# Kernel tuning notes

Measured on AMD Instinct MI355X. Metric: run time of the kernel, lower is better.

## Reference

```python
import jax, jax.numpy as jnp
import numpy as np

LN_EPS = 1e-5  # torch LayerNorm default
MODES = 4


def setup_inputs() -> dict:
    key = jax.random.key(0)
    ks = jax.random.split(key, 5)
    B, S, H = 4, 4096, 1024
    nh, dk = 16, H // 16
    scale = 1.0 / (H * H)
    # frequency mode selection: random shuffle of range(S//2), take 4, sorted (seeded for determinism)
    rng = np.random.default_rng(0)
    index = jnp.asarray(np.sort(rng.permutation(S // 2)[:MODES]).astype(np.int32))
    return {
        "x": jax.random.normal(ks[0], (B, S, H), dtype=jnp.float32),
        "Wq": jax.random.normal(ks[1], (H, H), dtype=jnp.float32) * np.sqrt(2.0 / (H + dk)),
        "bq": jnp.zeros((H,), dtype=jnp.float32),
        "wr": scale * jax.random.uniform(ks[2], (nh, dk, dk, MODES), dtype=jnp.float32),
        "wi": scale * jax.random.uniform(ks[3], (nh, dk, dk, MODES), dtype=jnp.float32),
        "gamma": jnp.ones((H,), dtype=jnp.float32),
        "beta": jnp.zeros((H,), dtype=jnp.float32),
        "index": index,
    }


def reference(x, Wq, bq, wr, wi, gamma, beta, index):
    B, S, H = x.shape
    nh, dk = wr.shape[0], wr.shape[1]
    # q projection and head split: (B,S,H) -> (B,S,nh,dk) -> (B,nh,dk,S)
    q = (x @ Wq.T + bq).reshape(B, S, nh, dk).transpose(0, 2, 3, 1)
    x_ft = jnp.fft.rfft(q, axis=-1)                 # (B,nh,dk,S//2+1) complex
    xm = x_ft[..., index]                           # gather selected modes: (B,nh,dk,M)
    w = wr + 1j * wi                                # (nh,dk,dk,M) complex
    ym = jnp.einsum('bhim,hiom->bhom', xm, w)       # per-mode complex matmul
    # faithful: results written at slots 0..M-1 of out_ft (loop writes out_ft[...,wi])
    out_ft = jnp.zeros((B, nh, dk, S // 2 + 1), dtype=ym.dtype).at[..., :ym.shape[-1]].set(ym)
    x_if = jnp.fft.irfft(out_ft, n=S, axis=-1)      # (B,nh,dk,S) real
    # faithful permute(0,3,2,1).view: flattens as dk-major over heads
    out = x_if.transpose(0, 3, 2, 1).reshape(B, S, H)
    # dropout is identity in eval mode
    y = out + x
    mu = jnp.mean(y, axis=-1, keepdims=True)
    var = jnp.var(y, axis=-1, keepdims=True)
    return (y - mu) * jax.lax.rsqrt(var + LN_EPS) * gamma + beta
```

## Files before the change

kernel.cpp:

```cpp
#include <hip/hip_runtime.h>
#include <math.h>

#define BB 4
#define SS 4096
#define HH 1024
#define NH 16
#define DK 64
#define NMODES 4
#define TWO_PI 6.28318530717958647692f

__global__ __launch_bounds__(512) void kA_dft(const float* __restrict__ x,
                                              const int* __restrict__ index,
                                              float* __restrict__ Gp) {
    __shared__ float tab[1024 * 8];
    __shared__ float red[8][16][33];
    int t   = threadIdx.x;
    int bid = blockIdx.x;
    int cb  = bid & 15;
    int sq  = (bid >> 4) & 3;
    int b   = bid >> 6;

    int k0 = index[0], k1 = index[1], k2 = index[2], k3 = index[3];
    for (int u = t; u < 4096; u += 512) {
        int sl = u >> 2, m = u & 3;
        int k  = (m == 0) ? k0 : (m == 1) ? k1 : (m == 2) ? k2 : k3;
        int sv = sq * 1024 + sl;
        int r  = (k * sv) & (SS - 1);
        float ang = (float)r * (TWO_PI / (float)SS);
        float sn, cs;
        sincosf(ang, &sn, &cs);
        tab[sl * 8 + m * 2]     = cs;
        tab[sl * 8 + m * 2 + 1] = sn;
    }
    __syncthreads();

    int c4 = t & 15, srow = t >> 4;
    int c0 = cb * 64 + c4 * 4;
    float acc[4][8];
    #pragma unroll
    for (int e = 0; e < 4; ++e)
        #pragma unroll
        for (int q = 0; q < 8; ++q) acc[e][q] = 0.f;

    const float* xp = x + ((size_t)(b * SS + sq * 1024 + srow)) * HH + c0;
    #pragma unroll 8
    for (int pass = 0; pass < 32; ++pass) {
        float4 xv = *(const float4*)(xp + (size_t)pass * 32 * HH);
        int sl = pass * 32 + srow;
        float4 t0 = *(const float4*)&tab[sl * 8];
        float4 t1 = *(const float4*)&tab[sl * 8 + 4];
        float xe;
        #pragma unroll
        for (int e = 0; e < 4; ++e) {
            xe = (e == 0) ? xv.x : (e == 1) ? xv.y : (e == 2) ? xv.z : xv.w;
            acc[e][0] += xe * t0.x;  acc[e][1] -= xe * t0.y;
            acc[e][2] += xe * t0.z;  acc[e][3] -= xe * t0.w;
            acc[e][4] += xe * t1.x;  acc[e][5] -= xe * t1.y;
            acc[e][6] += xe * t1.z;  acc[e][7] -= xe * t1.w;
        }
    }
    #pragma unroll
    for (int e = 0; e < 4; ++e)
        #pragma unroll
        for (int q = 0; q < 8; ++q) {
            acc[e][q] += __shfl_xor(acc[e][q], 16);
            acc[e][q] += __shfl_xor(acc[e][q], 32);
        }
    int w = t >> 6, lane = t & 63;
    if (lane < 16) {
        #pragma unroll
        for (int e = 0; e < 4; ++e)
            #pragma unroll
            for (int q = 0; q < 8; ++q)
                red[w][lane][e * 8 + q] = acc[e][q];
    }
    __syncthreads();
    {
        int q = t >> 6, oc = t & 63;
        float s = 0.f;
        #pragma unroll
        for (int w2 = 0; w2 < 8; ++w2)
            s += red[w2][oc >> 2][(oc & 3) * 8 + q];
        Gp[((size_t)((b * 4 + sq) * 8 + q)) * HH + cb * 64 + oc] = s;
    }
}

__global__ __launch_bounds__(512) void kBC(const float* __restrict__ Gp,
                                           const float* __restrict__ Wq,
                                           const float* __restrict__ bq,
                                           const int* __restrict__ index,
                                           const float* __restrict__ wr,
                                           const float* __restrict__ wi,
                                           float* __restrict__ CF) {
    __shared__ float Gs[8 * HH];
    __shared__ float xs[DK * 8];
    __shared__ float red[8][DK][9];
    int t = threadIdx.x;
    int h = blockIdx.x & 15;
    int b = blockIdx.x >> 4;

    {
        const float4* g0 = (const float4*)(Gp + (size_t)(b * 4 + 0) * 8 * HH);
        const float4* g1 = (const float4*)(Gp + (size_t)(b * 4 + 1) * 8 * HH);
        const float4* g2 = (const float4*)(Gp + (size_t)(b * 4 + 2) * 8 * HH);
        const float4* g3 = (const float4*)(Gp + (size_t)(b * 4 + 3) * 8 * HH);
        float4* gd = (float4*)Gs;
        for (int u = t; u < 2 * HH; u += 512) {
            float4 a = g0[u], b2 = g1[u], c = g2[u], d = g3[u];
            gd[u] = make_float4(a.x + b2.x + c.x + d.x,
                                a.y + b2.y + c.y + d.y,
                                a.z + b2.z + c.z + d.z,
                                a.w + b2.w + c.w + d.w);
        }
    }
    __syncthreads();

    {
        int cl = t >> 3, jq = t & 7;
        int c = h * DK + cl;
        float acc[8] = {0.f,0.f,0.f,0.f,0.f,0.f,0.f,0.f};
        for (int j0 = jq * 4; j0 < HH; j0 += 32) {
            float4 wv = *(const float4*)&Wq[(size_t)c * HH + j0];
            #pragma unroll
            for (int q = 0; q < 8; ++q) {
                float4 gv = *(const float4*)&Gs[q * HH + j0];
                acc[q] += wv.x * gv.x + wv.y * gv.y + wv.z * gv.z + wv.w * gv.w;
            }
        }
        #pragma unroll
        for (int q = 0; q < 8; ++q) {
            acc[q] += __shfl_xor(acc[q], 1);
            acc[q] += __shfl_xor(acc[q], 2);
            acc[q] += __shfl_xor(acc[q], 4);
        }
        if (jq == 0) {
            float bias = bq[c];
            #pragma unroll
            for (int m = 0; m < NMODES; ++m)
                if (index[m] == 0) acc[2 * m] += bias * (float)SS;
            #pragma unroll
            for (int q = 0; q < 8; ++q) xs[cl * 8 + q] = acc[q];
        }
    }
    __syncthreads();

    {
        int o = t & 63, iq = t >> 6;
        float re[4] = {0.f,0.f,0.f,0.f}, im[4] = {0.f,0.f,0.f,0.f};
        #pragma unroll
        for (int ii = 0; ii < 8; ++ii) {
            int i = iq * 8 + ii;
            float4 wrv = *(const float4*)&wr[(((size_t)(h * DK + i)) * DK + o) * 4];
            float4 wiv = *(const float4*)&wi[(((size_t)(h * DK + i)) * DK + o) * 4];
            float xr, xi;
            xr = xs[i * 8 + 0]; xi = xs[i * 8 + 1];
            re[0] += xr * wrv.x - xi * wiv.x;  im[0] += xr * wiv.x + xi * wrv.x;
            xr = xs[i * 8 + 2]; xi = xs[i * 8 + 3];
            re[1] += xr * wrv.y - xi * wiv.y;  im[1] += xr * wiv.y + xi * wrv.y;
            xr = xs[i * 8 + 4]; xi = xs[i * 8 + 5];
            re[2] += xr * wrv.z - xi * wiv.z;  im[2] += xr * wiv.z + xi * wrv.z;
            xr = xs[i * 8 + 6]; xi = xs[i * 8 + 7];
            re[3] += xr * wrv.w - xi * wiv.w;  im[3] += xr * wiv.w + xi * wrv.w;
        }
        #pragma unroll
        for (int m = 0; m < 4; ++m) {
            red[iq][o][2 * m]     = re[m];
            red[iq][o][2 * m + 1] = im[m];
        }
        __syncthreads();
        if (iq == 0) {
            float rr[8];
            #pragma unroll
            for (int q = 0; q < 8; ++q) {
                float s = 0.f;
                #pragma unroll
                for (int g = 0; g < 8; ++g) s += red[g][o][q];
                rr[q] = s;
            }
            int co = o * NH + h;
            const float inv = 1.0f / (float)SS;
            float* cp = CF + ((size_t)(b * HH + co)) * 8;
            cp[0] =  rr[0] * inv;
            cp[1] =  2.0f * rr[2] * inv;
            cp[2] = -2.0f * rr[3] * inv;
            cp[3] =  2.0f * rr[4] * inv;
            cp[4] = -2.0f * rr[5] * inv;
            cp[5] =  2.0f * rr[6] * inv;
            cp[6] = -2.0f * rr[7] * inv;
            cp[7] =  0.0f;
        }
    }
}

#define KD_ROWS 8
__global__ __launch_bounds__(256) void kD_out(const float* __restrict__ x,
                                              const float* __restrict__ CF,
                                              const float* __restrict__ gamma,
                                              const float* __restrict__ beta,
                                              float* __restrict__ out) {
    __shared__ float red[4][KD_ROWS][2];
    int t  = threadIdx.x;
    int b  = blockIdx.x >> 9;
    int s0 = (blockIdx.x & 511) * KD_ROWS;
    int c0 = t * 4;

    float myc, mys;
    {
        float ang = (float)(s0 + (t & 7)) * (TWO_PI / (float)SS);
        sincosf(ang, &mys, &myc);
    }

    const float* cp = CF + (size_t)b * HH * 8 + (size_t)c0 * 8;
    float4 cfa[8];
    #pragma unroll
    for (int e = 0; e < 4; ++e) {
        cfa[2 * e]     = *(const float4*)(cp + e * 8);
        cfa[2 * e + 1] = *(const float4*)(cp + e * 8 + 4);
    }
    float4 g4 = *(const float4*)&gamma[c0];
    float4 b4 = *(const float4*)&beta[c0];
    int w = t >> 6, lane = t & 63;

    float4 yv[KD_ROWS];
    #pragma unroll
    for (int r = 0; r < KD_ROWS; ++r) {
        int s = s0 + r;
        yv[r] = *(const float4*)&x[((size_t)(b * SS + s)) * HH + c0];
    }
    float sm[KD_ROWS], sq[KD_ROWS];
    #pragma unroll
    for (int r = 0; r < KD_ROWS; ++r) {
        float c1 = __shfl(myc, r), s1 = __shfl(mys, r);
        float c2 = c1 * c1 - s1 * s1, s2 = 2.f * s1 * c1;
        float c3 = c2 * c1 - s2 * s1, s3 = s2 * c1 + c2 * s1;
        float ye[4];
        #pragma unroll
        for (int e = 0; e < 4; ++e) {
            float xe = (e == 0) ? yv[r].x : (e == 1) ? yv[r].y
                     : (e == 2) ? yv[r].z : yv[r].w;
            float4 A = cfa[2 * e], Bv = cfa[2 * e + 1];
            ye[e] = xe + A.x + A.y * c1 + A.z * s1 + A.w * c2
                       + Bv.x * s2 + Bv.y * c3 + Bv.z * s3;
        }
        yv[r] = make_float4(ye[0], ye[1], ye[2], ye[3]);
        sm[r] = ye[0] + ye[1] + ye[2] + ye[3];
        sq[r] = ye[0]*ye[0] + ye[1]*ye[1] + ye[2]*ye[2] + ye[3]*ye[3];
    }
    #pragma unroll
    for (int off = 1; off < 64; off <<= 1) {
        #pragma unroll
        for (int r = 0; r < KD_ROWS; ++r) {
            sm[r] += __shfl_xor(sm[r], off);
            sq[r] += __shfl_xor(sq[r], off);
        }
    }
    if (lane == 0) {
        #pragma unroll
        for (int r = 0; r < KD_ROWS; ++r) {
            red[w][r][0] = sm[r];
            red[w][r][1] = sq[r];
        }
    }
    __syncthreads();
    #pragma unroll
    for (int r = 0; r < KD_ROWS; ++r) {
        int s = s0 + r;
        float tot  = red[0][r][0] + red[1][r][0] + red[2][r][0] + red[3][r][0];
        float totq = red[0][r][1] + red[1][r][1] + red[2][r][1] + red[3][r][1];
        float mean = tot * (1.0f / (float)HH);
        float var  = totq * (1.0f / (float)HH) - mean * mean;
        float rs = rsqrtf(var + 1e-5f);
        float4 o4;
        o4.x = (yv[r].x - mean) * rs * g4.x + b4.x;
        o4.y = (yv[r].y - mean) * rs * g4.y + b4.y;
        o4.z = (yv[r].z - mean) * rs * g4.z + b4.z;
        o4.w = (yv[r].w - mean) * rs * g4.w + b4.w;
        *(float4*)&out[((size_t)(b * SS + s)) * HH + c0] = o4;
    }
}

extern "C" void kernel_launch(void* const* d_in, const int* in_sizes, int n_in,
                              void* d_out, int out_size, void* d_ws, size_t ws_size,
                              hipStream_t stream) {
    const float* x     = (const float*)d_in[0];
    const float* Wq    = (const float*)d_in[1];
    const float* bq    = (const float*)d_in[2];
    const float* wr    = (const float*)d_in[3];
    const float* wi    = (const float*)d_in[4];
    const float* gamma = (const float*)d_in[5];
    const float* beta  = (const float*)d_in[6];
    const int*   index = (const int*)d_in[7];
    float* out = (float*)d_out;
    float* ws  = (float*)d_ws;

    const size_t nGp = (size_t)BB * 4 * 8 * HH;
    const size_t nCF = (size_t)BB * HH * 8;

    float *Gp, *CFb;
    if (ws_size >= (nGp + nCF) * sizeof(float)) {
        Gp  = ws;
        CFb = ws + nGp;
    } else {
        Gp  = out;
        CFb = ws;
    }

    hipLaunchKernelGGL(kA_dft, dim3(BB * 64), dim3(512), 0, stream, x, index, Gp);
    hipLaunchKernelGGL(kBC,    dim3(BB * NH), dim3(512), 0, stream,
                       Gp, Wq, bq, index, wr, wi, CFb);
    hipLaunchKernelGGL(kD_out, dim3(BB * (SS / KD_ROWS)), dim3(256), 0, stream,
                       x, CFb, gamma, beta, out);
}
```

Before: 60.54 us.

## Split DFT reduction into many sequence chunks with partial-sum planes, reduce in kBC

The first kernel now runs one block per 32-row sequence chunk, and each thread owns four full columns. It writes per-chunk partial DFT sums into eight planes instead of doing an intra-block shuffle and shared-memory reduction. kBC then sums the 128 partials per batch when it loads Gs. The output kernel hoists its x loads earlier and uses nontemporal stores. This trades a larger partial-sum buffer (16 MB written then read) and a heavier reduction in the 64-block kBC for removing the in-block reductions and spreading the DFT over more blocks.

```diff
diff --git a/kernel.cpp b/kernel.cpp
--- a/kernel.cpp
+++ b/kernel.cpp
@@ -7,24 +7,25 @@
 #define NH 16
 #define DK 64
 #define NMODES 4
+#define NSB 128
+#define SCHUNK (SS/NSB)
+#define PPLANE ((size_t)BB * NSB * HH)
 #define TWO_PI 6.28318530717958647692f
 
-__global__ __launch_bounds__(512) void kA_dft(const float* __restrict__ x,
+typedef float nfloat4 __attribute__((ext_vector_type(4)));
+
+__global__ __launch_bounds__(256) void kA_dft(const float* __restrict__ x,
                                               const int* __restrict__ index,
-                                              float* __restrict__ Gp) {
-    __shared__ float tab[1024 * 8];
-    __shared__ float red[8][16][33];
-    int t   = threadIdx.x;
-    int bid = blockIdx.x;
-    int cb  = bid & 15;
-    int sq  = (bid >> 4) & 3;
-    int b   = bid >> 6;
-
-    int k0 = index[0], k1 = index[1], k2 = index[2], k3 = index[3];
-    for (int u = t; u < 4096; u += 512) {
-        int sl = u >> 2, m = u & 3;
-        int k  = (m == 0) ? k0 : (m == 1) ? k1 : (m == 2) ? k2 : k3;
-        int sv = sq * 1024 + sl;
+                                              float* __restrict__ P) {
+    __shared__ float tab[SCHUNK * 8];
+    int t  = threadIdx.x;
+    int sb = blockIdx.x & (NSB - 1);
+    int b  = blockIdx.x >> 7;
+
+    if (t < SCHUNK * NMODES) {
+        int sl = t >> 2, m = t & 3;
+        int k  = index[m];
+        int sv = sb * SCHUNK + sl;
         int r  = (k * sv) & (SS - 1);
         float ang = (float)r * (TWO_PI / (float)SS);
         float sn, cs;
@@ -34,21 +35,19 @@
     }
     __syncthreads();
 
-    int c4 = t & 15, srow = t >> 4;
-    int c0 = cb * 64 + c4 * 4;
+    int c0 = t * 4;
     float acc[4][8];
     #pragma unroll
     for (int e = 0; e < 4; ++e)
         #pragma unroll
         for (int q = 0; q < 8; ++q) acc[e][q] = 0.f;
 
-    const float* xp = x + ((size_t)(b * SS + sq * 1024 + srow)) * HH + c0;
+    const float* xp = x + ((size_t)(b * SS + sb * SCHUNK)) * HH + c0;
     #pragma unroll 8
-    for (int pass = 0; pass < 32; ++pass) {
-        float4 xv = *(const float4*)(xp + (size_t)pass * 32 * HH);
-        int sl = pass * 32 + srow;
-        float4 t0 = *(const float4*)&tab[sl * 8];
-        float4 t1 = *(const float4*)&tab[sl * 8 + 4];
+    for (int r = 0; r < SCHUNK; ++r) {
+        float4 xv = *(const float4*)(xp + (size_t)r * HH);
+        float4 t0 = *(const float4*)&tab[r * 8];
+        float4 t1 = *(const float4*)&tab[r * 8 + 4];
         float xe;
         #pragma unroll
         for (int e = 0; e < 4; ++e) {
@@ -59,33 +58,15 @@
             acc[e][6] += xe * t1.z;  acc[e][7] -= xe * t1.w;
         }
     }
-    #pragma unroll
-    for (int e = 0; e < 4; ++e)
-        #pragma unroll
-        for (int q = 0; q < 8; ++q) {
-            acc[e][q] += __shfl_xor(acc[e][q], 16);
-            acc[e][q] += __shfl_xor(acc[e][q], 32);
-        }
-    int w = t >> 6, lane = t & 63;
-    if (lane < 16) {
-        #pragma unroll
-        for (int e = 0; e < 4; ++e)
-            #pragma unroll
-            for (int q = 0; q < 8; ++q)
-                red[w][lane][e * 8 + q] = acc[e][q];
-    }
-    __syncthreads();
-    {
-        int q = t >> 6, oc = t & 63;
-        float s = 0.f;
-        #pragma unroll
-        for (int w2 = 0; w2 < 8; ++w2)
-            s += red[w2][oc >> 2][(oc & 3) * 8 + q];
-        Gp[((size_t)((b * 4 + sq) * 8 + q)) * HH + cb * 64 + oc] = s;
+    size_t base = (size_t)(b * NSB + sb) * HH + c0;
+    #pragma unroll
+    for (int q = 0; q < 8; ++q) {
+        *(float4*)&P[q * PPLANE + base] =
+            make_float4(acc[0][q], acc[1][q], acc[2][q], acc[3][q]);
     }
 }
 
-__global__ __launch_bounds__(512) void kBC(const float* __restrict__ Gp,
+__global__ __launch_bounds__(512) void kBC(const float* __restrict__ P,
                                            const float* __restrict__ Wq,
                                            const float* __restrict__ bq,
                                            const int* __restrict__ index,
@@ -100,17 +81,32 @@
     int b = blockIdx.x >> 4;
 
     {
-        const float4* g0 = (const float4*)(Gp + (size_t)(b * 4 + 0) * 8 * HH);
-        const float4* g1 = (const float4*)(Gp + (size_t)(b * 4 + 1) * 8 * HH);
-        const float4* g2 = (const float4*)(Gp + (size_t)(b * 4 + 2) * 8 * HH);
-        const float4* g3 = (const float4*)(Gp + (size_t)(b * 4 + 3) * 8 * HH);
-        float4* gd = (float4*)Gs;
-        for (int u = t; u < 2 * HH; u += 512) {
-            float4 a = g0[u], b2 = g1[u], c = g2[u], d = g3[u];
-            gd[u] = make_float4(a.x + b2.x + c.x + d.x,
-                                a.y + b2.y + c.y + d.y,
-                                a.z + b2.z + c.z + d.z,
-                                a.w + b2.w + c.w + d.w);
+        int oq = t >> 6, jg = t & 63;
+        #pragma unroll
+        for (int k = 0; k < 4; ++k) {
+            int j0 = (jg + 64 * k) * 4;
+            const float4* pp = (const float4*)(P + (size_t)oq * PPLANE
+                             + (size_t)b * NSB * HH + j0);
+            float4 s0 = make_float4(0.f, 0.f, 0.f, 0.f);
+            float4 s1 = make_float4(0.f, 0.f, 0.f, 0.f);
+            float4 s2 = make_float4(0.f, 0.f, 0.f, 0.f);
+            float4 s3 = make_float4(0.f, 0.f, 0.f, 0.f);
+            #pragma unroll 4
+            for (int sb = 0; sb < NSB; sb += 4) {
+                float4 v0 = pp[(size_t)(sb + 0) * (HH / 4)];
+                float4 v1 = pp[(size_t)(sb + 1) * (HH / 4)];
+                float4 v2 = pp[(size_t)(sb + 2) * (HH / 4)];
+                float4 v3 = pp[(size_t)(sb + 3) * (HH / 4)];
+                s0.x += v0.x; s0.y += v0.y; s0.z += v0.z; s0.w += v0.w;
+                s1.x += v1.x; s1.y += v1.y; s1.z += v1.z; s1.w += v1.w;
+                s2.x += v2.x; s2.y += v2.y; s2.z += v2.z; s2.w += v2.w;
+                s3.x += v3.x; s3.y += v3.y; s3.z += v3.z; s3.w += v3.w;
+            }
+            float4 s = make_float4((s0.x + s1.x) + (s2.x + s3.x),
+                                   (s0.y + s1.y) + (s2.y + s3.y),
+                                   (s0.z + s1.z) + (s2.z + s3.z),
+                                   (s0.w + s1.w) + (s2.w + s3.w));
+            *(float4*)&Gs[oq * HH + j0] = s;
         }
     }
     __syncthreads();
@@ -203,6 +199,14 @@
     int b  = blockIdx.x >> 9;
     int s0 = (blockIdx.x & 511) * KD_ROWS;
     int c0 = t * 4;
+    int w = t >> 6, lane = t & 63;
+
+    float4 yv[KD_ROWS];
+    #pragma unroll
+    for (int r = 0; r < KD_ROWS; ++r) {
+        int s = s0 + r;
+        yv[r] = *(const float4*)&x[((size_t)(b * SS + s)) * HH + c0];
+    }
 
     float myc, mys;
     {
@@ -219,14 +223,7 @@
     }
     float4 g4 = *(const float4*)&gamma[c0];
     float4 b4 = *(const float4*)&beta[c0];
-    int w = t >> 6, lane = t & 63;
-
-    float4 yv[KD_ROWS];
-    #pragma unroll
-    for (int r = 0; r < KD_ROWS; ++r) {
-        int s = s0 + r;
-        yv[r] = *(const float4*)&x[((size_t)(b * SS + s)) * HH + c0];
-    }
+
     float sm[KD_ROWS], sq[KD_ROWS];
     #pragma unroll
     for (int r = 0; r < KD_ROWS; ++r) {
@@ -270,12 +267,13 @@
         float mean = tot * (1.0f / (float)HH);
         float var  = totq * (1.0f / (float)HH) - mean * mean;
         float rs = rsqrtf(var + 1e-5f);
-        float4 o4;
+        nfloat4 o4;
         o4.x = (yv[r].x - mean) * rs * g4.x + b4.x;
         o4.y = (yv[r].y - mean) * rs * g4.y + b4.y;
         o4.z = (yv[r].z - mean) * rs * g4.z + b4.z;
         o4.w = (yv[r].w - mean) * rs * g4.w + b4.w;
-        *(float4*)&out[((size_t)(b * SS + s)) * HH + c0] = o4;
+        __builtin_nontemporal_store(o4,
+            (nfloat4*)&out[((size_t)(b * SS + s)) * HH + c0]);
     }
 }
 
@@ -293,21 +291,21 @@
     float* out = (float*)d_out;
     float* ws  = (float*)d_ws;
 
-    const size_t nGp = (size_t)BB * 4 * 8 * HH;
+    const size_t nP  = PPLANE * 8;
     const size_t nCF = (size_t)BB * HH * 8;
 
-    float *Gp, *CFb;
-    if (ws_size >= (nGp + nCF) * sizeof(float)) {
-        Gp  = ws;
-        CFb = ws + nGp;
+    float *P, *CFb;
+    if (ws_size >= (nP + nCF) * sizeof(float)) {
+        P   = ws;
+        CFb = ws + nP;
     } else {
-        Gp  = out;
+        P   = out;
         CFb = ws;
     }
 
-    hipLaunchKernelGGL(kA_dft, dim3(BB * 64), dim3(512), 0, stream, x, index, Gp);
+    hipLaunchKernelGGL(kA_dft, dim3(BB * NSB), dim3(256), 0, stream, x, index, P);
     hipLaunchKernelGGL(kBC,    dim3(BB * NH), dim3(512), 0, stream,
-                       Gp, Wq, bq, index, wr, wi, CFb);
+                       P, Wq, bq, index, wr, wi, CFb);
     hipLaunchKernelGGL(kD_out, dim3(BB * (SS / KD_ROWS)), dim3(256), 0, stream,
                        x, CFb, gamma, beta, out);
 }
```

New measurement: 95.47 us. 57.7% more time.
